# Kernel tuning notes

Hardware: AMD Instinct MI355X
Metric: run time of the kernel (lower is better)

## Reference

```python
import jax, jax.numpy as jnp
import numpy as np

N, n, m, k = 100000, 32, 16, 32
MU = 100.0  # bubble kernel scale (init arg mu)


def setup_inputs() -> dict:
    key = jax.random.key(0)
    ks = jax.random.split(key, 7)
    x = jax.random.normal(ks[0], (N,), dtype=jnp.float32)
    # torch.nn.Linear(N, n): weight [n, N], bias [n]
    encoder_w = jax.random.normal(ks[1], (n, N), dtype=jnp.float32) / np.float32(np.sqrt(N))
    encoder_b = jnp.zeros((n,), dtype=jnp.float32)
    # decoder parameter [n, N]
    decoder = jax.random.normal(ks[2], (n, N), dtype=jnp.float32) / np.float32(np.sqrt(n))
    # torch.nn.Linear(n, n*m): weight [n*m, n], bias [n*m]
    bw_w = jax.random.normal(ks[3], (n * m, n), dtype=jnp.float32) / np.float32(np.sqrt(n))
    bw_b = jnp.zeros((n * m,), dtype=jnp.float32)
    neighbour_distance = jax.random.uniform(ks[4], (N, k), dtype=jnp.float32)
    neighbour_id = jax.random.randint(ks[5], (N, k), 0, N)
    clustering_labels = jax.random.randint(ks[6], (N,), 0, m)
    return {
        "x": x,
        "encoder_w": encoder_w,
        "encoder_b": encoder_b,
        "decoder": decoder,
        "bw_w": bw_w,
        "bw_b": bw_b,
        "neighbour_distance": neighbour_distance,
        "neighbour_id": neighbour_id,
        "clustering_labels": clustering_labels,
    }


def reference(x, encoder_w, encoder_b, decoder, bw_w, bw_b,
              neighbour_distance, neighbour_id, clustering_labels):
    # encode: [N] -> [n]
    encoded = x @ encoder_w.T + encoder_b
    # per-basis, per-cluster bandwidths: sigmoid(Linear)/60 -> [n, m] -> expand to [n, N]
    bandwidths = jax.nn.sigmoid(encoded @ bw_w.T + bw_b) / 60.0
    w = bandwidths.reshape(n, m)[:, clustering_labels]  # [n, N]
    # bubble window: relu(1 - d^2 / (w*mu)^2) -> [n, N, k]
    window = jax.nn.relu(1.0 - neighbour_distance[None, :, :] ** 2
                         / (w[:, :, None] * MU) ** 2)
    # normalization over axis 1 (the N axis), faithful to the source's dim=1
    window = window / jnp.sum(window, axis=1, keepdims=True)
    # gather decoder rows at neighbours, weight, reduce over k: [n, N]
    convolved_basis = jnp.sum(decoder[:, neighbour_id] * window, axis=-1)
    # [n] @ [n, N] -> [N]
    return encoded @ convolved_basis
```

## Files before the change

### kernel.cpp

```cpp
#include <hip/hip_runtime.h>
#include <hip/hip_fp16.h>

#define N_PTS 100000
#define MU_F  100.0f

typedef unsigned int uint;
typedef _Float16 h2 __attribute__((ext_vector_type(2)));
typedef float f2 __attribute__((ext_vector_type(2)));

#define E_SCALE 16384.0f
#define E_SCALE_INV (1.0f / 16384.0f)

static __device__ inline h2 h2pack(float a, float b) {
    return __builtin_bit_cast(h2, __builtin_amdgcn_cvt_pkrtz(a, b));
}
static __device__ inline float fdot2f(h2 a, h2 b, float c) {
    return __builtin_amdgcn_fdot2(a, b, c, false);
}
static __device__ inline h2 h2fma(h2 a, h2 b, h2 c) {
#if __has_builtin(__builtin_elementwise_fma)
    return __builtin_elementwise_fma(a, b, c);
#else
    return a * b + c;
#endif
}
static __device__ inline h2 h2max(h2 a, h2 b) {
#if __has_builtin(__builtin_elementwise_max)
    return __builtin_elementwise_max(a, b);
#else
    h2 r;
    r.x = a.x > b.x ? a.x : b.x;
    r.y = a.y > b.y ? a.y : b.y;
    return r;
#endif
}

#define ENC_BLKS 256
#define TR_BLKS  1563
#define S_BLKS   1024
#define S_PCH    98
#define S_PAD    104
#define NCOPY    8
#define NPAIRS   (N_PTS / 2)
#define M_BLKS   1024
#define M_CH     49


__global__ __launch_bounds__(256) void k_prep_tr(const float* __restrict__ x,
                                                 const float* __restrict__ encW,
                                                 const float* __restrict__ encB,
                                                 float* __restrict__ enc,
                                                 const float* __restrict__ dec,
                                                 __half* __restrict__ decT) {
    int b = blockIdx.x;
    if (b < ENC_BLKS) {
        int row = b & 31;
        int chunk = b >> 5;
        const int CH = N_PTS / 8;
        int base = chunk * CH;
        const float4* W4 = reinterpret_cast<const float4*>(encW + (size_t)row * N_PTS + base);
        const float4* x4 = reinterpret_cast<const float4*>(x + base);
        const int nv = CH / 4;
        float acc = 0.f;
        for (int idx = threadIdx.x; idx < nv; idx += 256) {
            float4 w = W4[idx];
            float4 xv = x4[idx];
            acc += w.x * xv.x + w.y * xv.y + w.z * xv.z + w.w * xv.w;
        }
        #pragma unroll
        for (int off = 32; off > 0; off >>= 1) acc += __shfl_down(acc, off);
        __shared__ float sred[4];
        int wid = threadIdx.x >> 6;
        if ((threadIdx.x & 63) == 0) sred[wid] = acc;
        __syncthreads();
        if (threadIdx.x == 0) {
            float s = sred[0] + sred[1] + sred[2] + sred[3];
            if (chunk == 0) s += encB[row];
            atomicAdd(enc + row, s);
        }
    } else {
        __shared__ float tile[32][65];
        int j0 = (b - ENC_BLKS) * 64;
        int col = threadIdx.x & 63;
        int r0 = threadIdx.x >> 6;
        #pragma unroll
        for (int it = 0; it < 8; ++it) {
            int row = it * 4 + r0;
            int j = j0 + col;
            float v = (j < N_PTS) ? dec[(size_t)row * N_PTS + j] : 0.f;
            tile[row][col] = v;
        }
        __syncthreads();
        #pragma unroll
        for (int it = 0; it < 4; ++it) {
            int idx = it * 256 + threadIdx.x;
            int j = idx >> 4;
            int p = idx & 15;
            int jj = j0 + j;
            if (jj < N_PTS) {
                __half2 h = __halves2half2(__float2half(tile[2 * p][j]),
                                           __float2half(tile[2 * p + 1][j]));
                *reinterpret_cast<__half2*>(decT + (size_t)jj * 32 + 2 * p) = h;
            }
        }
    }
}

__global__ __launch_bounds__(256) void k_tab(const float* __restrict__ enc_g,
                                             const float* __restrict__ bw_w,
                                             const float* __restrict__ bw_b,
                                             float* __restrict__ invFG,
                                             h2* __restrict__ invHLG) {
    __shared__ float encL[32];
    __shared__ float invF[512];
    if (threadIdx.x < 32) encL[threadIdx.x] = enc_g[threadIdx.x];
    __syncthreads();
    for (int r = threadIdx.x; r < 512; r += 256) {
        int i = r >> 4, c = r & 15;
        const float4* wr4 = reinterpret_cast<const float4*>(bw_w + (size_t)r * 32);
        float z = bw_b[r];
        #pragma unroll
        for (int p4 = 0; p4 < 8; ++p4) {
            float4 wv = wr4[p4];
            z = fmaf(encL[4 * p4 + 0], wv.x, z);
            z = fmaf(encL[4 * p4 + 1], wv.y, z);
            z = fmaf(encL[4 * p4 + 2], wv.z, z);
            z = fmaf(encL[4 * p4 + 3], wv.w, z);
        }
        float s = 1.f / (1.f + __expf(-z));
        float wmu = s * (MU_F / 60.0f);
        float iv = 1.f / (wmu * wmu);
        invF[c * 32 + i] = iv;
        invFG[c * 32 + i] = iv;
    }
    __syncthreads();
    {
        int t = threadIdx.x;
        int c = t >> 4, q = (t >> 2) & 3, tt = t & 3;
        int i0 = q * 8 + 2 * tt;
        invHLG[t] = h2pack(fminf(invF[c * 32 + i0], 6.0e4f),
                           fminf(invF[c * 32 + i0 + 1], 6.0e4f));
    }
}

__global__ __launch_bounds__(256, 8) void k_S(const float* __restrict__ invFG,
                                              const float* __restrict__ nd,
                                              const int* __restrict__ labels,
                                              float* __restrict__ S8) {
    __shared__ float invF[512];
    __shared__ int   labL[S_PAD];
    __shared__ float pInv[S_PAD * 32];
    int t = threadIdx.x;
    int start = blockIdx.x * S_PCH;
    int jend = min(start + S_PCH, N_PTS);
    int npts = jend - start;

    if (t < 128)
        reinterpret_cast<float4*>(invF)[t] =
            reinterpret_cast<const float4*>(invFG)[t];
    if (npts > 0 && t < S_PAD) {
        int jc = min(t, npts - 1);
        labL[t] = labels[start + jc];
    }
    __syncthreads();
    if (npts > 0) {
        for (int e = t; e < S_PAD * 32; e += 256) {
            int j = e >> 5, kk = e & 31;
            pInv[e] = invF[labL[j] * 32 + kk];
        }
    }
    __syncthreads();
    if (npts <= 0) return;

    int kk = t & 31;
    int ig = t >> 5;
    float a0 = 0.f, a1 = 0.f, a2 = 0.f, a3 = 0.f;

    auto ld4d = [&](int jbase, float* d) {
        #pragma unroll
        for (int u = 0; u < 4; ++u) {
            int j = jbase + u;
            int jc = min(j, N_PTS - 1);
            float dv = __builtin_nontemporal_load(&nd[(size_t)jc * 32 + kk]);
            d[u] = (j < jend) ? dv : 1.0e15f;
        }
    };
    float dA[4], dB[4], dC[4];
    ld4d(start, dA);
    ld4d(start + 4, dB);
    for (int jj = start; jj < jend; jj += 4) {
        ld4d(jj + 8, dC);
        int base = (jj - start) * 32 + ig * 4;
        #pragma unroll
        for (int u = 0; u < 4; ++u) {
            float4 iv = *reinterpret_cast<const float4*>(&pInv[base + u * 32]);
            float d2 = dA[u] * dA[u];
            a0 += fmaxf(fmaf(d2, -iv.x, 1.f), 0.f);
            a1 += fmaxf(fmaf(d2, -iv.y, 1.f), 0.f);
            a2 += fmaxf(fmaf(d2, -iv.z, 1.f), 0.f);
            a3 += fmaxf(fmaf(d2, -iv.w, 1.f), 0.f);
        }
        #pragma unroll
        for (int u = 0; u < 4; ++u) { dA[u] = dB[u]; dB[u] = dC[u]; }
    }

    float* Sc = S8 + (size_t)(blockIdx.x & (NCOPY - 1)) * 1024;
    int cell = (ig * 4) * 32 + kk;
    atomicAdd(&Sc[cell], a0);
    atomicAdd(&Sc[cell + 32], a1);
    atomicAdd(&Sc[cell + 64], a2);
    atomicAdd(&Sc[cell + 96], a3);
}

__global__ __launch_bounds__(256, 4) void k_main(const h2* __restrict__ invHLG,
                                                 const float* __restrict__ enc_g,
                                                 const float* __restrict__ S8,
                                                 const float* __restrict__ nd,
                                                 const int* __restrict__ nid,
                                                 const int* __restrict__ labels,
                                                 const __half* __restrict__ decT,
                                                 float* __restrict__ out) {
    __shared__ h2 invHL[256];
    __shared__ float Sred[1024];
    if (threadIdx.x < 64)
        reinterpret_cast<uint4*>(invHL)[threadIdx.x] =
            reinterpret_cast<const uint4*>(invHLG)[threadIdx.x];
    for (int t = threadIdx.x; t < 1024; t += 256) {
        float s = 0.f;
        #pragma unroll
        for (int c = 0; c < NCOPY; ++c)
            s += S8[(size_t)c * 1024 + t];
        Sred[t] = s;
    }
    __syncthreads();

    int lane = threadIdx.x & 63;
    int R = lane >> 2;
    int q = lane & 3;

    h2 EhA[4], EhB[4];
    #pragma unroll
    for (int t = 0; t < 4; ++t) {
        int i0 = q * 8 + 2 * t;
        float e0 = enc_g[i0], e1 = enc_g[i0 + 1];
        float sA0 = Sred[i0 * 32 + R],      sA1 = Sred[(i0 + 1) * 32 + R];
        float sB0 = Sred[i0 * 32 + R + 16], sB1 = Sred[(i0 + 1) * 32 + R + 16];
        EhA[t] = h2pack(e0 / sA0 * E_SCALE, e1 / sA1 * E_SCALE);
        EhB[t] = h2pack(e0 / sB0 * E_SCALE, e1 / sB1 * E_SCALE);
    }
    const h2 zero2 = h2pack(0.f, 0.f);
    const h2 one2 = h2pack(1.f, 1.f);

    int w = threadIdx.x >> 6;
    int start = blockIdx.x * M_CH;
    int pend = min(start + M_CH, NPAIRS);
    const uint4* decQ = reinterpret_cast<const uint4*>(decT);

    auto load_ldd = [&](int jp0, int jp1, int* id, float* dd) {
        #pragma unroll
        for (int s = 0; s < 4; ++s) {
            size_t idx = (size_t)((s >> 1) ? jp1 : jp0) * 32 + (s & 1) * 16 + R;
            id[s] = __builtin_nontemporal_load(&nid[idx]);
            dd[s] = __builtin_nontemporal_load(&nd[idx]);
        }
    };
    auto load_ih = [&](int c0, int c1, h2* ih0, h2* ih1) {
        uint4 a = *reinterpret_cast<const uint4*>(&invHL[c0 * 16 + q * 4]);
        uint4 bq = *reinterpret_cast<const uint4*>(&invHL[c1 * 16 + q * 4]);
        ih0[0] = __builtin_bit_cast(h2, a.x);  ih0[1] = __builtin_bit_cast(h2, a.y);
        ih0[2] = __builtin_bit_cast(h2, a.z);  ih0[3] = __builtin_bit_cast(h2, a.w);
        ih1[0] = __builtin_bit_cast(h2, bq.x); ih1[1] = __builtin_bit_cast(h2, bq.y);
        ih1[2] = __builtin_bit_cast(h2, bq.z); ih1[3] = __builtin_bit_cast(h2, bq.w);
    };

    for (int p = start + w; p < pend; p += 8) {
        bool has2 = (p + 4) < pend;
        int p2 = has2 ? (p + 4) : p;
        int jA0 = 2 * p,  jA1 = jA0 + 1;
        int jB0 = 2 * p2, jB1 = jB0 + 1;

        int cA0 = labels[jA0], cA1 = labels[jA1];
        int cB0 = labels[jB0], cB1 = labels[jB1];
        int idA[4], idB[4]; float ddA[4], ddB[4];
        load_ldd(jA0, jA1, idA, ddA);
        load_ldd(jB0, jB1, idB, ddB);
        uint4 rA[4], rB[4];
        #pragma unroll
        for (int s = 0; s < 4; ++s) {
            rA[s] = decQ[(size_t)idA[s] * 4 + q];
            rB[s] = decQ[(size_t)idB[s] * 4 + q];
        }
        h2 ihA0[4], ihA1[4], ihB0[4], ihB1[4];
        load_ih(cA0, cA1, ihA0, ihA1);
        load_ih(cB0, cB1, ihB0, ihB1);

        h2 mdA0, mdA1, mdA2, mdA3, mdB0, mdB1, mdB2, mdB3;
        {
            float d0 = ddA[0] * ddA[0], d1 = ddA[1] * ddA[1];
            float d2 = ddA[2] * ddA[2], d3 = ddA[3] * ddA[3];
            mdA0 = h2pack(-d0, -d0); mdA1 = h2pack(-d1, -d1);
            mdA2 = h2pack(-d2, -d2); mdA3 = h2pack(-d3, -d3);
            float e0 = ddB[0] * ddB[0], e1 = ddB[1] * ddB[1];
            float e2 = ddB[2] * ddB[2], e3 = ddB[3] * ddB[3];
            mdB0 = h2pack(-e0, -e0); mdB1 = h2pack(-e1, -e1);
            mdB2 = h2pack(-e2, -e2); mdB3 = h2pack(-e3, -e3);
        }

        float a0 = 0.f, a1 = 0.f, a2 = 0.f, a3 = 0.f;
        float b0 = 0.f, b1 = 0.f, b2 = 0.f, b3 = 0.f;
        #pragma unroll
        for (int t = 0; t < 4; ++t) {
            uint wA0 = (t == 0) ? rA[0].x : (t == 1) ? rA[0].y : (t == 2) ? rA[0].z : rA[0].w;
            uint wA1 = (t == 0) ? rA[1].x : (t == 1) ? rA[1].y : (t == 2) ? rA[1].z : rA[1].w;
            uint wA2 = (t == 0) ? rA[2].x : (t == 1) ? rA[2].y : (t == 2) ? rA[2].z : rA[2].w;
            uint wA3 = (t == 0) ? rA[3].x : (t == 1) ? rA[3].y : (t == 2) ? rA[3].z : rA[3].w;
            uint wB0 = (t == 0) ? rB[0].x : (t == 1) ? rB[0].y : (t == 2) ? rB[0].z : rB[0].w;
            uint wB1 = (t == 0) ? rB[1].x : (t == 1) ? rB[1].y : (t == 2) ? rB[1].z : rB[1].w;
            uint wB2 = (t == 0) ? rB[2].x : (t == 1) ? rB[2].y : (t == 2) ? rB[2].z : rB[2].w;
            uint wB3 = (t == 0) ? rB[3].x : (t == 1) ? rB[3].y : (t == 2) ? rB[3].z : rB[3].w;
            {
                h2 wv = h2max(h2fma(mdA0, ihA0[t], one2), zero2);
                a0 = fdot2f(wv * EhA[t], __builtin_bit_cast(h2, wA0), a0);
            }
            {
                h2 wv = h2max(h2fma(mdA1, ihA0[t], one2), zero2);
                a1 = fdot2f(wv * EhB[t], __builtin_bit_cast(h2, wA1), a1);
            }
            {
                h2 wv = h2max(h2fma(mdA2, ihA1[t], one2), zero2);
                a2 = fdot2f(wv * EhA[t], __builtin_bit_cast(h2, wA2), a2);
            }
            {
                h2 wv = h2max(h2fma(mdA3, ihA1[t], one2), zero2);
                a3 = fdot2f(wv * EhB[t], __builtin_bit_cast(h2, wA3), a3);
            }
            {
                h2 wv = h2max(h2fma(mdB0, ihB0[t], one2), zero2);
                b0 = fdot2f(wv * EhA[t], __builtin_bit_cast(h2, wB0), b0);
            }
            {
                h2 wv = h2max(h2fma(mdB1, ihB0[t], one2), zero2);
                b1 = fdot2f(wv * EhB[t], __builtin_bit_cast(h2, wB1), b1);
            }
            {
                h2 wv = h2max(h2fma(mdB2, ihB1[t], one2), zero2);
                b2 = fdot2f(wv * EhA[t], __builtin_bit_cast(h2, wB2), b2);
            }
            {
                h2 wv = h2max(h2fma(mdB3, ihB1[t], one2), zero2);
                b3 = fdot2f(wv * EhB[t], __builtin_bit_cast(h2, wB3), b3);
            }
        }
        float u = a0 + a1;
        float v = a2 + a3;
        float u2 = b0 + b1;
        float v2 = b2 + b3;
        #pragma unroll
        for (int off = 32; off > 0; off >>= 1) {
            u += __shfl_xor(u, off);
            v += __shfl_xor(v, off);
            u2 += __shfl_xor(u2, off);
            v2 += __shfl_xor(v2, off);
        }
        if (lane == 0) {
            out[jA0] = u * E_SCALE_INV;
            if (has2) out[jB0] = u2 * E_SCALE_INV;
        }
        if (lane == 32) {
            out[jA1] = v * E_SCALE_INV;
            if (has2) out[jB1] = v2 * E_SCALE_INV;
        }
    }
}

extern "C" void kernel_launch(void* const* d_in, const int* in_sizes, int n_in,
                              void* d_out, int out_size, void* d_ws, size_t ws_size,
                              hipStream_t stream) {
    const float* x     = (const float*)d_in[0];
    const float* enc_w = (const float*)d_in[1];
    const float* enc_b = (const float*)d_in[2];
    const float* dec   = (const float*)d_in[3];
    const float* bw_w  = (const float*)d_in[4];
    const float* bw_b  = (const float*)d_in[5];
    const float* nd    = (const float*)d_in[6];
    const int*   nid   = (const int*)d_in[7];
    const int*   labels= (const int*)d_in[8];
    float* out = (float*)d_out;

    char* ws = (char*)d_ws;
    float* enc    = (float*)(ws + 0);
    float* S8     = (float*)(ws + 128);
    float* invFG  = (float*)(ws + 32896);
    h2*    invHLG = (h2*)(ws + 34944);
    __half* decT  = (__half*)(ws + 532480);

    (void)hipMemsetAsync(d_ws, 0, 32896, stream);
    k_prep_tr<<<dim3(ENC_BLKS + TR_BLKS), dim3(256), 0, stream>>>(
        x, enc_w, enc_b, enc, dec, decT);
    k_tab<<<dim3(1), dim3(256), 0, stream>>>(enc, bw_w, bw_b, invFG, invHLG);
    k_S<<<dim3(S_BLKS), dim3(256), 0, stream>>>(invFG, nd, labels, S8);
    k_main<<<dim3(M_BLKS), dim3(256), 0, stream>>>(invHLG, enc, S8, nd, nid,
                                                   labels, decT, out);
}
```

Measured before the change: 168.5 us.

## Split transposed decoder into two half-basis tables and gather in two passes

The fp16 transposed decoder is stored as two separate tables, one for basis rows 0-15 and one for rows 16-31. The main kernel now runs two passes over its points, each gathering from only one half, and combines the partial sums through shared memory. Each pass's random-gather working set halves, which is meant to fit better in L2 and cut the cost of random gathers. In exchange, neighbour ids, distances and labels are re-read in the second pass, and loop and reduction overhead doubles.

After: 189.6 us. +12.5%, slower.

```diff
diff --git a/kernel.cpp b/kernel.cpp
--- a/kernel.cpp
+++ b/kernel.cpp
@@ -51,7 +51,8 @@
                                                  const float* __restrict__ encB,
                                                  float* __restrict__ enc,
                                                  const float* __restrict__ dec,
-                                                 __half* __restrict__ decT) {
+                                                 __half* __restrict__ decL,
+                                                 __half* __restrict__ decH) {
     int b = blockIdx.x;
     if (b < ENC_BLKS) {
         int row = b & 31;
@@ -100,7 +101,9 @@
             if (jj < N_PTS) {
                 __half2 h = __halves2half2(__float2half(tile[2 * p][j]),
                                            __float2half(tile[2 * p + 1][j]));
-                *reinterpret_cast<__half2*>(decT + (size_t)jj * 32 + 2 * p) = h;
+                __half* dst = (p < 8) ? (decL + (size_t)jj * 16 + 2 * p)
+                                      : (decH + (size_t)jj * 16 + 2 * (p - 8));
+                *reinterpret_cast<__half2*>(dst) = h;
             }
         }
     }
@@ -110,7 +113,7 @@
                                              const float* __restrict__ bw_w,
                                              const float* __restrict__ bw_b,
                                              float* __restrict__ invFG,
-                                             h2* __restrict__ invHLG) {
+                                             h2* __restrict__ invHLG2) {
     __shared__ float encL[32];
     __shared__ float invF[512];
     if (threadIdx.x < 32) encL[threadIdx.x] = enc_g[threadIdx.x];
@@ -136,10 +139,10 @@
     __syncthreads();
     {
         int t = threadIdx.x;
-        int c = t >> 4, q = (t >> 2) & 3, tt = t & 3;
-        int i0 = q * 8 + 2 * tt;
-        invHLG[t] = h2pack(fminf(invF[c * 32 + i0], 6.0e4f),
-                           fminf(invF[c * 32 + i0 + 1], 6.0e4f));
+        int hh = t >> 7, c = (t >> 3) & 15, qq = (t >> 1) & 3, t2 = t & 1;
+        int i0 = hh * 16 + qq * 4 + 2 * t2;
+        invHLG2[t] = h2pack(fminf(invF[c * 32 + i0], 6.0e4f),
+                            fminf(invF[c * 32 + i0 + 1], 6.0e4f));
     }
 }
 
@@ -212,19 +215,21 @@
     atomicAdd(&Sc[cell + 96], a3);
 }
 
-__global__ __launch_bounds__(256, 4) void k_main(const h2* __restrict__ invHLG,
+__global__ __launch_bounds__(256, 4) void k_main(const h2* __restrict__ invHLG2,
                                                  const float* __restrict__ enc_g,
                                                  const float* __restrict__ S8,
                                                  const float* __restrict__ nd,
                                                  const int* __restrict__ nid,
                                                  const int* __restrict__ labels,
-                                                 const __half* __restrict__ decT,
+                                                 const __half* __restrict__ decL,
+                                                 const __half* __restrict__ decH,
                                                  float* __restrict__ out) {
-    __shared__ h2 invHL[256];
+    __shared__ h2 invHL2[256];
     __shared__ float Sred[1024];
+    __shared__ float part[2 * M_CH + 8];
     if (threadIdx.x < 64)
-        reinterpret_cast<uint4*>(invHL)[threadIdx.x] =
-            reinterpret_cast<const uint4*>(invHLG)[threadIdx.x];
+        reinterpret_cast<uint4*>(invHL2)[threadIdx.x] =
+            reinterpret_cast<const uint4*>(invHLG2)[threadIdx.x];
     for (int t = threadIdx.x; t < 1024; t += 256) {
         float s = 0.f;
         #pragma unroll
@@ -238,15 +243,20 @@
     int R = lane >> 2;
     int q = lane & 3;
 
-    h2 EhA[4], EhB[4];
+    h2 EA0[2], EB0[2], EA1[2], EB1[2];
     #pragma unroll
-    for (int t = 0; t < 4; ++t) {
-        int i0 = q * 8 + 2 * t;
-        float e0 = enc_g[i0], e1 = enc_g[i0 + 1];
-        float sA0 = Sred[i0 * 32 + R],      sA1 = Sred[(i0 + 1) * 32 + R];
-        float sB0 = Sred[i0 * 32 + R + 16], sB1 = Sred[(i0 + 1) * 32 + R + 16];
-        EhA[t] = h2pack(e0 / sA0 * E_SCALE, e1 / sA1 * E_SCALE);
-        EhB[t] = h2pack(e0 / sB0 * E_SCALE, e1 / sB1 * E_SCALE);
+    for (int hh = 0; hh < 2; ++hh) {
+        #pragma unroll
+        for (int t2 = 0; t2 < 2; ++t2) {
+            int i0 = hh * 16 + q * 4 + 2 * t2;
+            float e0 = enc_g[i0], e1 = enc_g[i0 + 1];
+            float sA0 = Sred[i0 * 32 + R],      sA1 = Sred[(i0 + 1) * 32 + R];
+            float sB0 = Sred[i0 * 32 + R + 16], sB1 = Sred[(i0 + 1) * 32 + R + 16];
+            h2 ea = h2pack(e0 / sA0 * E_SCALE, e1 / sA1 * E_SCALE);
+            h2 eb = h2pack(e0 / sB0 * E_SCALE, e1 / sB1 * E_SCALE);
+            if (hh == 0) { EA0[t2] = ea; EB0[t2] = eb; }
+            else         { EA1[t2] = ea; EB1[t2] = eb; }
+        }
     }
     const h2 zero2 = h2pack(0.f, 0.f);
     const h2 one2 = h2pack(1.f, 1.f);
@@ -254,7 +264,6 @@
     int w = threadIdx.x >> 6;
     int start = blockIdx.x * M_CH;
     int pend = min(start + M_CH, NPAIRS);
-    const uint4* decQ = reinterpret_cast<const uint4*>(decT);
 
     auto load_ldd = [&](int jp0, int jp1, int* id, float* dd) {
         #pragma unroll
@@ -264,113 +273,126 @@
             dd[s] = __builtin_nontemporal_load(&nd[idx]);
         }
     };
-    auto load_ih = [&](int c0, int c1, h2* ih0, h2* ih1) {
-        uint4 a = *reinterpret_cast<const uint4*>(&invHL[c0 * 16 + q * 4]);
-        uint4 bq = *reinterpret_cast<const uint4*>(&invHL[c1 * 16 + q * 4]);
-        ih0[0] = __builtin_bit_cast(h2, a.x);  ih0[1] = __builtin_bit_cast(h2, a.y);
-        ih0[2] = __builtin_bit_cast(h2, a.z);  ih0[3] = __builtin_bit_cast(h2, a.w);
-        ih1[0] = __builtin_bit_cast(h2, bq.x); ih1[1] = __builtin_bit_cast(h2, bq.y);
-        ih1[2] = __builtin_bit_cast(h2, bq.z); ih1[3] = __builtin_bit_cast(h2, bq.w);
+
+    auto run_pass = [&](const uint2* decQ2, const h2* ihTab,
+                        const h2* EA, const h2* EB, bool first) {
+        for (int p = start + w; p < pend; p += 8) {
+            bool has2 = (p + 4) < pend;
+            int p2 = has2 ? (p + 4) : p;
+            int jA0 = 2 * p,  jA1 = jA0 + 1;
+            int jB0 = 2 * p2, jB1 = jB0 + 1;
+
+            int cA0 = labels[jA0], cA1 = labels[jA1];
+            int cB0 = labels[jB0], cB1 = labels[jB1];
+            int idA[4], idB[4]; float ddA[4], ddB[4];
+            load_ldd(jA0, jA1, idA, ddA);
+            load_ldd(jB0, jB1, idB, ddB);
+            uint2 rA[4], rB[4];
+            #pragma unroll
+            for (int s = 0; s < 4; ++s) {
+                rA[s] = decQ2[(size_t)idA[s] * 4 + q];
+                rB[s] = decQ2[(size_t)idB[s] * 4 + q];
+            }
+            h2 ihA0[2], ihA1[2], ihB0[2], ihB1[2];
+            {
+                uint2 a = *reinterpret_cast<const uint2*>(&ihTab[cA0 * 8 + q * 2]);
+                uint2 b2 = *reinterpret_cast<const uint2*>(&ihTab[cA1 * 8 + q * 2]);
+                uint2 cc = *reinterpret_cast<const uint2*>(&ihTab[cB0 * 8 + q * 2]);
+                uint2 dd2 = *reinterpret_cast<const uint2*>(&ihTab[cB1 * 8 + q * 2]);
+                ihA0[0] = __builtin_bit_cast(h2, a.x);  ihA0[1] = __builtin_bit_cast(h2, a.y);
+                ihA1[0] = __builtin_bit_cast(h2, b2.x); ihA1[1] = __builtin_bit_cast(h2, b2.y);
+                ihB0[0] = __builtin_bit_cast(h2, cc.x); ihB0[1] = __builtin_bit_cast(h2, cc.y);
+                ihB1[0] = __builtin_bit_cast(h2, dd2.x); ihB1[1] = __builtin_bit_cast(h2, dd2.y);
+            }
+
+            h2 mdA0, mdA1, mdA2, mdA3, mdB0, mdB1, mdB2, mdB3;
+            {
+                float d0 = ddA[0] * ddA[0], d1 = ddA[1] * ddA[1];
+                float d2 = ddA[2] * ddA[2], d3 = ddA[3] * ddA[3];
+                mdA0 = h2pack(-d0, -d0); mdA1 = h2pack(-d1, -d1);
+                mdA2 = h2pack(-d2, -d2); mdA3 = h2pack(-d3, -d3);
+                float e0 = ddB[0] * ddB[0], e1 = ddB[1] * ddB[1];
+                float e2 = ddB[2] * ddB[2], e3 = ddB[3] * ddB[3];
+                mdB0 = h2pack(-e0, -e0); mdB1 = h2pack(-e1, -e1);
+                mdB2 = h2pack(-e2, -e2); mdB3 = h2pack(-e3, -e3);
+            }
+
+            float a0 = 0.f, a1 = 0.f, a2 = 0.f, a3 = 0.f;
+            float b0 = 0.f, b1 = 0.f, b2 = 0.f, b3 = 0.f;
+            #pragma unroll
+            for (int t2 = 0; t2 < 2; ++t2) {
+                uint wA0 = t2 ? rA[0].y : rA[0].x;
+                uint wA1 = t2 ? rA[1].y : rA[1].x;
+                uint wA2 = t2 ? rA[2].y : rA[2].x;
+                uint wA3 = t2 ? rA[3].y : rA[3].x;
+                uint wB0 = t2 ? rB[0].y : rB[0].x;
+                uint wB1 = t2 ? rB[1].y : rB[1].x;
+                uint wB2 = t2 ? rB[2].y : rB[2].x;
+                uint wB3 = t2 ? rB[3].y : rB[3].x;
+                {
+                    h2 wv = h2max(h2fma(mdA0, ihA0[t2], one2), zero2);
+                    a0 = fdot2f(wv * EA[t2], __builtin_bit_cast(h2, wA0), a0);
+                }
+                {
+                    h2 wv = h2max(h2fma(mdA1, ihA0[t2], one2), zero2);
+                    a1 = fdot2f(wv * EB[t2], __builtin_bit_cast(h2, wA1), a1);
+                }
+                {
+                    h2 wv = h2max(h2fma(mdA2, ihA1[t2], one2), zero2);
+                    a2 = fdot2f(wv * EA[t2], __builtin_bit_cast(h2, wA2), a2);
+                }
+                {
+                    h2 wv = h2max(h2fma(mdA3, ihA1[t2], one2), zero2);
+                    a3 = fdot2f(wv * EB[t2], __builtin_bit_cast(h2, wA3), a3);
+                }
+                {
+                    h2 wv = h2max(h2fma(mdB0, ihB0[t2], one2), zero2);
+                    b0 = fdot2f(wv * EA[t2], __builtin_bit_cast(h2, wB0), b0);
+                }
+                {
+                    h2 wv = h2max(h2fma(mdB1, ihB0[t2], one2), zero2);
+                    b1 = fdot2f(wv * EB[t2], __builtin_bit_cast(h2, wB1), b1);
+                }
+                {
+                    h2 wv = h2max(h2fma(mdB2, ihB1[t2], one2), zero2);
+                    b2 = fdot2f(wv * EA[t2], __builtin_bit_cast(h2, wB2), b2);
+                }
+                {
+                    h2 wv = h2max(h2fma(mdB3, ihB1[t2], one2), zero2);
+                    b3 = fdot2f(wv * EB[t2], __builtin_bit_cast(h2, wB3), b3);
+                }
+            }
+            float u = a0 + a1;
+            float v = a2 + a3;
+            float u2 = b0 + b1;
+            float v2 = b2 + b3;
+            #pragma unroll
+            for (int off = 32; off > 0; off >>= 1) {
+                u += __shfl_xor(u, off);
+                v += __shfl_xor(v, off);
+                u2 += __shfl_xor(u2, off);
+                v2 += __shfl_xor(v2, off);
+            }
+            int ia = jA0 - 2 * start;
+            int ib = jB0 - 2 * start;
+            if (first) {
+                if (lane == 0)  { part[ia] = u;      part[ib] = u2; }
+                if (lane == 32) { part[ia + 1] = v;  part[ib + 1] = v2; }
+            } else {
+                if (lane == 0) {
+                    out[jA0] = (u + part[ia]) * E_SCALE_INV;
+                    if (has2) out[jB0] = (u2 + part[ib]) * E_SCALE_INV;
+                }
+                if (lane == 32) {
+                    out[jA1] = (v + part[ia + 1]) * E_SCALE_INV;
+                    if (has2) out[jB1] = (v2 + part[ib + 1]) * E_SCALE_INV;
+                }
+            }
+        }
     };
 
-    for (int p = start + w; p < pend; p += 8) {
-        bool has2 = (p + 4) < pend;
-        int p2 = has2 ? (p + 4) : p;
-        int jA0 = 2 * p,  jA1 = jA0 + 1;
-        int jB0 = 2 * p2, jB1 = jB0 + 1;
-
-        int cA0 = labels[jA0], cA1 = labels[jA1];
-        int cB0 = labels[jB0], cB1 = labels[jB1];
-        int idA[4], idB[4]; float ddA[4], ddB[4];
-        load_ldd(jA0, jA1, idA, ddA);
-        load_ldd(jB0, jB1, idB, ddB);
-        uint4 rA[4], rB[4];
-        #pragma unroll
-        for (int s = 0; s < 4; ++s) {
-            rA[s] = decQ[(size_t)idA[s] * 4 + q];
-            rB[s] = decQ[(size_t)idB[s] * 4 + q];
-        }
-        h2 ihA0[4], ihA1[4], ihB0[4], ihB1[4];
-        load_ih(cA0, cA1, ihA0, ihA1);
-        load_ih(cB0, cB1, ihB0, ihB1);
-
-        h2 mdA0, mdA1, mdA2, mdA3, mdB0, mdB1, mdB2, mdB3;
-        {
-            float d0 = ddA[0] * ddA[0], d1 = ddA[1] * ddA[1];
-            float d2 = ddA[2] * ddA[2], d3 = ddA[3] * ddA[3];
-            mdA0 = h2pack(-d0, -d0); mdA1 = h2pack(-d1, -d1);
-            mdA2 = h2pack(-d2, -d2); mdA3 = h2pack(-d3, -d3);
-            float e0 = ddB[0] * ddB[0], e1 = ddB[1] * ddB[1];
-            float e2 = ddB[2] * ddB[2], e3 = ddB[3] * ddB[3];
-            mdB0 = h2pack(-e0, -e0); mdB1 = h2pack(-e1, -e1);
-            mdB2 = h2pack(-e2, -e2); mdB3 = h2pack(-e3, -e3);
-        }
-
-        float a0 = 0.f, a1 = 0.f, a2 = 0.f, a3 = 0.f;
-        float b0 = 0.f, b1 = 0.f, b2 = 0.f, b3 = 0.f;
-        #pragma unroll
-        for (int t = 0; t < 4; ++t) {
-            uint wA0 = (t == 0) ? rA[0].x : (t == 1) ? rA[0].y : (t == 2) ? rA[0].z : rA[0].w;
-            uint wA1 = (t == 0) ? rA[1].x : (t == 1) ? rA[1].y : (t == 2) ? rA[1].z : rA[1].w;
-            uint wA2 = (t == 0) ? rA[2].x : (t == 1) ? rA[2].y : (t == 2) ? rA[2].z : rA[2].w;
-            uint wA3 = (t == 0) ? rA[3].x : (t == 1) ? rA[3].y : (t == 2) ? rA[3].z : rA[3].w;
-            uint wB0 = (t == 0) ? rB[0].x : (t == 1) ? rB[0].y : (t == 2) ? rB[0].z : rB[0].w;
-            uint wB1 = (t == 0) ? rB[1].x : (t == 1) ? rB[1].y : (t == 2) ? rB[1].z : rB[1].w;
-            uint wB2 = (t == 0) ? rB[2].x : (t == 1) ? rB[2].y : (t == 2) ? rB[2].z : rB[2].w;
-            uint wB3 = (t == 0) ? rB[3].x : (t == 1) ? rB[3].y : (t == 2) ? rB[3].z : rB[3].w;
-            {
-                h2 wv = h2max(h2fma(mdA0, ihA0[t], one2), zero2);
-                a0 = fdot2f(wv * EhA[t], __builtin_bit_cast(h2, wA0), a0);
-            }
-            {
-                h2 wv = h2max(h2fma(mdA1, ihA0[t], one2), zero2);
-                a1 = fdot2f(wv * EhB[t], __builtin_bit_cast(h2, wA1), a1);
-            }
-            {
-                h2 wv = h2max(h2fma(mdA2, ihA1[t], one2), zero2);
-                a2 = fdot2f(wv * EhA[t], __builtin_bit_cast(h2, wA2), a2);
-            }
-            {
-                h2 wv = h2max(h2fma(mdA3, ihA1[t], one2), zero2);
-                a3 = fdot2f(wv * EhB[t], __builtin_bit_cast(h2, wA3), a3);
-            }
-            {
-                h2 wv = h2max(h2fma(mdB0, ihB0[t], one2), zero2);
-                b0 = fdot2f(wv * EhA[t], __builtin_bit_cast(h2, wB0), b0);
-            }
-            {
-                h2 wv = h2max(h2fma(mdB1, ihB0[t], one2), zero2);
-                b1 = fdot2f(wv * EhB[t], __builtin_bit_cast(h2, wB1), b1);
-            }
-            {
-                h2 wv = h2max(h2fma(mdB2, ihB1[t], one2), zero2);
-                b2 = fdot2f(wv * EhA[t], __builtin_bit_cast(h2, wB2), b2);
-            }
-            {
-                h2 wv = h2max(h2fma(mdB3, ihB1[t], one2), zero2);
-                b3 = fdot2f(wv * EhB[t], __builtin_bit_cast(h2, wB3), b3);
-            }
-        }
-        float u = a0 + a1;
-        float v = a2 + a3;
-        float u2 = b0 + b1;
-        float v2 = b2 + b3;
-        #pragma unroll
-        for (int off = 32; off > 0; off >>= 1) {
-            u += __shfl_xor(u, off);
-            v += __shfl_xor(v, off);
-            u2 += __shfl_xor(u2, off);
-            v2 += __shfl_xor(v2, off);
-        }
-        if (lane == 0) {
-            out[jA0] = u * E_SCALE_INV;
-            if (has2) out[jB0] = u2 * E_SCALE_INV;
-        }
-        if (lane == 32) {
-            out[jA1] = v * E_SCALE_INV;
-            if (has2) out[jB1] = v2 * E_SCALE_INV;
-        }
-    }
+    run_pass(reinterpret_cast<const uint2*>(decL), invHL2,       EA0, EB0, true);
+    run_pass(reinterpret_cast<const uint2*>(decH), invHL2 + 128, EA1, EB1, false);
 }
 
 extern "C" void kernel_launch(void* const* d_in, const int* in_sizes, int n_in,
@@ -388,17 +410,18 @@
     float* out = (float*)d_out;
 
     char* ws = (char*)d_ws;
-    float* enc    = (float*)(ws + 0);
-    float* S8     = (float*)(ws + 128);
-    float* invFG  = (float*)(ws + 32896);
-    h2*    invHLG = (h2*)(ws + 34944);
-    __half* decT  = (__half*)(ws + 532480);
+    float* enc     = (float*)(ws + 0);
+    float* S8      = (float*)(ws + 128);
+    float* invFG   = (float*)(ws + 32896);
+    h2*    invHLG2 = (h2*)(ws + 34944);
+    __half* decL   = (__half*)(ws + 532480);
+    __half* decH   = (__half*)(ws + 3732480);
 
     (void)hipMemsetAsync(d_ws, 0, 32896, stream);
     k_prep_tr<<<dim3(ENC_BLKS + TR_BLKS), dim3(256), 0, stream>>>(
-        x, enc_w, enc_b, enc, dec, decT);
-    k_tab<<<dim3(1), dim3(256), 0, stream>>>(enc, bw_w, bw_b, invFG, invHLG);
+        x, enc_w, enc_b, enc, dec, decL, decH);
+    k_tab<<<dim3(1), dim3(256), 0, stream>>>(enc, bw_w, bw_b, invFG, invHLG2);
     k_S<<<dim3(S_BLKS), dim3(256), 0, stream>>>(invFG, nd, labels, S8);
-    k_main<<<dim3(M_BLKS), dim3(256), 0, stream>>>(invHLG, enc, S8, nd, nid,
-                                                   labels, decT, out);
-}
+    k_main<<<dim3(M_BLKS), dim3(256), 0, stream>>>(invHLG2, enc, S8, nd, nid,
+                                                   labels, decL, decH, out);
+}
```
